# Performance work log

Measured on AMD Instinct MI355X. Metric: run time of the kernel, lower is better.

## Reference

```python
import jax, jax.numpy as jnp
import numpy as np

DIM = 768
HEADS = 12
HEAD_DIM = DIM // HEADS


def setup_inputs() -> dict:
    key = jax.random.key(0)
    ks = jax.random.split(key, 5)
    B, S = 4, 2048
    init = 0.02
    x = jax.random.normal(ks[0], (B, S, DIM), dtype=jnp.float32)
    w_qkv = jax.random.normal(ks[1], (DIM, 3 * DIM), dtype=jnp.float32) * init
    b_qkv = jnp.zeros((3 * DIM,), dtype=jnp.float32)
    w_out = jax.random.normal(ks[2], (DIM, DIM), dtype=jnp.float32) * init
    b_out = jnp.zeros((DIM,), dtype=jnp.float32)
    return {"x": x, "w_qkv": w_qkv, "b_qkv": b_qkv, "w_out": w_out, "b_out": b_out}


def reference(x, w_qkv, b_qkv, w_out, b_out):
    B, S, D = x.shape
    # QKV projection: [B,S,3D] -> [3,B,H,S,hd]
    qkv = x @ w_qkv + b_qkv
    qkv = qkv.reshape(B, S, 3, HEADS, HEAD_DIM).transpose(2, 0, 3, 1, 4)
    q, k, v = qkv[0], qkv[1], qkv[2]
    # NOTE: original scales by 1/sqrt(head_num), not 1/sqrt(head_dim)
    scale = 1.0 / jnp.sqrt(jnp.float32(HEADS))
    scores = jnp.einsum("bhqd,bhkd->bhqk", q, k) * scale
    attn = jax.nn.softmax(scores, axis=-1)
    out = jnp.einsum("bhqk,bhkd->bhqd", attn, v)
    out = out.transpose(0, 2, 1, 3).reshape(B, S, D)
    return out @ w_out + b_out
```

## Files before the change

kernel.cpp:

```cpp
#include <hip/hip_runtime.h>
#include <hip/hip_bf16.h>
#include <cstdint>
#include <cstddef>

#define HEADS 12
#define HD    64
#define NB    4
#define SEQ   2048
#define DIM   768
#define NQKV  2304

static constexpr float QSCALE = 0.2886751345948129f * 1.4426950408889634f;

typedef __attribute__((ext_vector_type(8))) short short8;
typedef __attribute__((ext_vector_type(4))) short short4v;
typedef __attribute__((ext_vector_type(4))) float f32x4;

__device__ inline unsigned short f2bf(float x) {
    union { float f; uint32_t u; } v; v.f = x;
    return (unsigned short)((v.u + 0x7fffu + ((v.u >> 16) & 1u)) >> 16);
}

__device__ inline unsigned short f2bf_fast(float x) {
    __hip_bfloat16 h = __float2bfloat16(x);
    unsigned short u;
    __builtin_memcpy(&u, &h, 2);
    return u;
}

__device__ inline void gld16(const void* g, void* l) {
    __builtin_amdgcn_global_load_lds(
        (const __attribute__((address_space(1))) unsigned int*)g,
        (__attribute__((address_space(3))) unsigned int*)l, 16, 0, 0);
}

__device__ inline void transpose_tile(
    const float* __restrict__ w, unsigned short* __restrict__ wT,
    int ncols, int nrows, int bx, int by, float (*tile)[65])
{
    const int k0 = by * 64;
    const int n0 = bx * 64;
    const int tr = threadIdx.x >> 4;
    const int tc4 = (threadIdx.x & 15) * 4;
    #pragma unroll
    for (int it = 0; it < 4; ++it) {
        const int kk = tr + it * 16;
        *reinterpret_cast<float4*>(&tile[kk][tc4]) =
            *reinterpret_cast<const float4*>(w + (size_t)(k0 + kk) * ncols + n0 + tc4);
    }
    __syncthreads();
    #pragma unroll
    for (int it = 0; it < 4; ++it) {
        const int nn = tr + it * 16;
        short4v o;
        #pragma unroll
        for (int r = 0; r < 4; ++r) o[r] = (short)f2bf(tile[tc4 + r][nn]);
        *reinterpret_cast<short4v*>(wT + (size_t)(n0 + nn) * nrows + k0 + tc4) = o;
    }
}

__global__ __launch_bounds__(256) void prep_kernel(
    const float* __restrict__ x, unsigned short* __restrict__ xb,
    const float* __restrict__ wq, unsigned short* __restrict__ wqT,
    const float* __restrict__ wo, unsigned short* __restrict__ woT)
{
    __shared__ float tile[64][65];
    const int bid = blockIdx.x;
    if (bid < 3072) {
        const size_t i = ((size_t)bid * 256 + threadIdx.x) * 8;
        const float4 a = *reinterpret_cast<const float4*>(x + i);
        const float4 b = *reinterpret_cast<const float4*>(x + i + 4);
        short8 o;
        o[0] = (short)f2bf(a.x); o[1] = (short)f2bf(a.y);
        o[2] = (short)f2bf(a.z); o[3] = (short)f2bf(a.w);
        o[4] = (short)f2bf(b.x); o[5] = (short)f2bf(b.y);
        o[6] = (short)f2bf(b.z); o[7] = (short)f2bf(b.w);
        *reinterpret_cast<short8*>(xb + i) = o;
    } else if (bid < 3072 + 432) {
        const int r = bid - 3072;
        transpose_tile(wq, wqT, NQKV, DIM, r % 36, r / 36, tile);
    } else {
        const int r = bid - 3504;
        transpose_tile(wo, woT, DIM, DIM, r % 12, r / 12, tile);
    }
}

__global__ __launch_bounds__(512) void qkv_gemm_bf16(
    const unsigned short* __restrict__ A,
    const unsigned short* __restrict__ BT,
    const float* __restrict__ bias,
    unsigned short* __restrict__ qb, unsigned short* __restrict__ kb,
    unsigned short* __restrict__ vt)
{
    __shared__ __align__(16) unsigned short As[2][128][64];
    __shared__ __align__(16) unsigned short Bs[2][128][64];

    const int tid = threadIdx.x;
    const int wave = tid >> 6;
    const int lane = tid & 63;
    const int col = lane & 15;
    const int g = lane >> 4;
    const int m0 = blockIdx.y * 128;
    const int n0 = blockIdx.x * 128;
    const int wr = wave >> 2;
    const int wc = wave & 3;

    f32x4 acc[4][2] = {};

    auto STAGE = [&](int kt, int bsel) {
        #pragma unroll
        for (int it = 0; it < 2; ++it) {
            const int slot = tid + it * 512;
            const int row = slot >> 3;
            const int cg = (slot & 7) ^ (row & 7);
            gld16(A + (size_t)(m0 + row) * DIM + kt + cg * 8,
                  &As[bsel][0][0] + (size_t)slot * 8);
            gld16(BT + (size_t)(n0 + row) * DIM + kt + cg * 8,
                  &Bs[bsel][0][0] + (size_t)slot * 8);
        }
    };

    const int NKT = DIM / 64;
    STAGE(0, 0);
    asm volatile("s_waitcnt vmcnt(0)" ::: "memory");
    __builtin_amdgcn_s_barrier();

    for (int t = 0; t < NKT; ++t) {
        const int cur = t & 1;
        if (t + 1 < NKT) STAGE((t + 1) * 64, cur ^ 1);

        #pragma unroll
        for (int ks = 0; ks < 2; ++ks) {
            short8 af[4], bf[2];
            #pragma unroll
            for (int i = 0; i < 4; ++i) {
                const int ra = wr * 64 + i * 16 + col;
                af[i] = *reinterpret_cast<const short8*>(
                    &As[cur][ra][(((ks * 4 + g) ^ (ra & 7)) << 3)]);
            }
            #pragma unroll
            for (int j = 0; j < 2; ++j) {
                const int rb = wc * 32 + j * 16 + col;
                bf[j] = *reinterpret_cast<const short8*>(
                    &Bs[cur][rb][(((ks * 4 + g) ^ (rb & 7)) << 3)]);
            }
            #pragma unroll
            for (int i = 0; i < 4; ++i)
                #pragma unroll
                for (int j = 0; j < 2; ++j)
                    acc[i][j] = __builtin_amdgcn_mfma_f32_16x16x32_bf16(
                        af[i], bf[j], acc[i][j], 0, 0, 0);
        }

        if (t + 1 < NKT) {
            asm volatile("s_waitcnt vmcnt(0)" ::: "memory");
            __builtin_amdgcn_s_barrier();
        }
    }

    const int which = n0 / DIM;
    #pragma unroll
    for (int j = 0; j < 2; ++j) {
        const int n = n0 + wc * 32 + j * 16 + col;
        const int rem = n - which * DIM;
        const int h = rem >> 6, dh = rem & 63;
        const float bj = bias[n];
        #pragma unroll
        for (int i = 0; i < 4; ++i) {
            const int mbase = m0 + wr * 64 + i * 16 + g * 4;
            const int b_ = mbase >> 11;
            const int s_ = mbase & 2047;
            const size_t bh = (size_t)(b_ * HEADS + h);
            if (which == 2) {
                short4v pk;
                #pragma unroll
                for (int r = 0; r < 4; ++r)
                    pk[r] = (short)f2bf(acc[i][j][r] + bj);
                *reinterpret_cast<short4v*>(vt + (bh * HD + dh) * SEQ + s_) = pk;
            } else {
                unsigned short* dst = (which == 0) ? qb : kb;
                const float sc = (which == 0) ? QSCALE : 1.0f;
                #pragma unroll
                for (int r = 0; r < 4; ++r)
                    dst[(bh * SEQ + s_ + r) * HD + dh] =
                        f2bf((acc[i][j][r] + bj) * sc);
            }
        }
    }
}

__global__ __launch_bounds__(512) void attn_kernel(
    const unsigned short* __restrict__ qb, const unsigned short* __restrict__ kbuf,
    const unsigned short* __restrict__ vt, unsigned short* __restrict__ ctxb)
{
    __shared__ __align__(16) unsigned short Ks[2][64][64];
    __shared__ __align__(16) unsigned short Vs[2][64][64];
    __shared__ __align__(16) unsigned short Ps[8][16][64];

    const int tid = threadIdx.x;
    const int wave = tid >> 6;
    const int lane = tid & 63;
    const int col = lane & 15;
    const int g   = lane >> 4;

    const int bid = blockIdx.x;
    const int vbid = (bid & 7) * 96 + (bid >> 3);
    const int bh = vbid >> 4;
    const int q0 = (vbid & 15) * 128;
    const int wq = q0 + wave * 16 + col;

    const size_t hb = (size_t)bh * SEQ * HD;

    short8 qf[2];
    {
        const unsigned short* src = qb + hb + (size_t)wq * HD + g * 8;
        qf[0] = *reinterpret_cast<const short8*>(src);
        qf[1] = *reinterpret_cast<const short8*>(src + 32);
    }

    f32x4 acc4[4] = {};
    float l_part = 0.0f;

    const unsigned short* Kg = kbuf + hb;
    const unsigned short* Vg = vt + hb;

    const int srow = tid >> 3;
    const int scl  = tid & 7;
    const int scg  = scl ^ (srow & 7);

    auto STAGE = [&](int jt, int bsel) {
        const int kb0 = jt * 64;
        gld16(Kg + (size_t)(kb0 + srow) * HD + scg * 8,
              &Ks[bsel][0][0] + (size_t)tid * 8);
        gld16(Vg + (size_t)srow * SEQ + kb0 + scg * 8,
              &Vs[bsel][0][0] + (size_t)tid * 8);
    };

    const int NT = SEQ / 64;
    STAGE(0, 0);

    for (int jt = 0; jt < NT; ++jt) {
        const int cur = jt & 1;
        if (jt + 1 < NT) {
            STAGE(jt + 1, cur ^ 1);
            asm volatile("s_waitcnt vmcnt(2)" ::: "memory");
        } else {
            asm volatile("s_waitcnt vmcnt(0)" ::: "memory");
        }
        __builtin_amdgcn_s_barrier();

        f32x4 st[4] = {};
        __builtin_amdgcn_s_setprio(1);
        #pragma unroll
        for (int m = 0; m < 4; ++m) {
            const int row = m * 16 + col;
            const short8 kf0 = *reinterpret_cast<const short8*>(
                &Ks[cur][row][((g ^ (row & 7)) << 3)]);
            const short8 kf1 = *reinterpret_cast<const short8*>(
                &Ks[cur][row][(((g + 4) ^ (row & 7)) << 3)]);
            st[m] = __builtin_amdgcn_mfma_f32_16x16x32_bf16(kf0, qf[0], st[m], 0, 0, 0);
            st[m] = __builtin_amdgcn_mfma_f32_16x16x32_bf16(kf1, qf[1], st[m], 0, 0, 0);
        }
        __builtin_amdgcn_s_setprio(0);

        float s0 = 0.0f, s1 = 0.0f, s2 = 0.0f, s3 = 0.0f;
        #pragma unroll
        for (int m = 0; m < 4; ++m) {
            float p[4];
            p[0] = __builtin_amdgcn_exp2f(st[m][0]);
            p[1] = __builtin_amdgcn_exp2f(st[m][1]);
            p[2] = __builtin_amdgcn_exp2f(st[m][2]);
            p[3] = __builtin_amdgcn_exp2f(st[m][3]);
            s0 += p[0]; s1 += p[1]; s2 += p[2]; s3 += p[3];
            short4v pk;
            #pragma unroll
            for (int r = 0; r < 4; ++r) pk[r] = (short)f2bf_fast(p[r]);
            const int scw = (2 * m + (g >> 1)) ^ (col & 7);
            *reinterpret_cast<short4v*>(
                &Ps[wave][col][(scw << 3) + ((g & 1) << 2)]) = pk;
        }
        l_part += (s0 + s1) + (s2 + s3);

        const short8 pf0 = *reinterpret_cast<const short8*>(
            &Ps[wave][col][((g ^ (col & 7)) << 3)]);
        const short8 pf1 = *reinterpret_cast<const short8*>(
            &Ps[wave][col][(((g + 4) ^ (col & 7)) << 3)]);

        __builtin_amdgcn_s_setprio(1);
        #pragma unroll
        for (int nb = 0; nb < 4; ++nb) {
            const int row = nb * 16 + col;
            const short8 vf0 = *reinterpret_cast<const short8*>(
                &Vs[cur][row][((g ^ (row & 7)) << 3)]);
            const short8 vf1 = *reinterpret_cast<const short8*>(
                &Vs[cur][row][(((g + 4) ^ (row & 7)) << 3)]);
            acc4[nb] = __builtin_amdgcn_mfma_f32_16x16x32_bf16(pf0, vf0, acc4[nb], 0, 0, 0);
            acc4[nb] = __builtin_amdgcn_mfma_f32_16x16x32_bf16(pf1, vf1, acc4[nb], 0, 0, 0);
        }
        __builtin_amdgcn_s_setprio(0);

        __builtin_amdgcn_s_barrier();
    }

    float lt = l_part + __shfl_xor(l_part, 16);
    lt += __shfl_xor(lt, 32);
    float lr[4];
    #pragma unroll
    for (int r = 0; r < 4; ++r) lr[r] = 1.0f / __shfl(lt, g * 4 + r);
    const int b_ = bh / HEADS;
    const int h = bh - b_ * HEADS;
    #pragma unroll
    for (int nb = 0; nb < 4; ++nb)
        #pragma unroll
        for (int r = 0; r < 4; ++r) {
            const int s_ = q0 + wave * 16 + g * 4 + r;
            ctxb[((size_t)b_ * SEQ + s_) * DIM + h * HD + nb * 16 + col] =
                f2bf_fast(acc4[nb][r] * lr[r]);
        }
}

__global__ __launch_bounds__(512) void out_gemm_bf16(
    const unsigned short* __restrict__ A,
    const unsigned short* __restrict__ BT,
    const float* __restrict__ bias, float* __restrict__ out)
{
    __shared__ __align__(16) unsigned short As[2][128][64];
    __shared__ __align__(16) unsigned short Bs[2][128][64];

    const int tid = threadIdx.x;
    const int wave = tid >> 6;
    const int lane = tid & 63;
    const int col = lane & 15;
    const int g = lane >> 4;
    const int m0 = blockIdx.y * 128;
    const int n0 = blockIdx.x * 128;
    const int wr = wave >> 2;
    const int wc = wave & 3;

    f32x4 acc[4][2] = {};

    auto STAGE = [&](int kt, int bsel) {
        #pragma unroll
        for (int it = 0; it < 2; ++it) {
            const int slot = tid + it * 512;
            const int row = slot >> 3;
            const int cg = (slot & 7) ^ (row & 7);
            gld16(A + (size_t)(m0 + row) * DIM + kt + cg * 8,
                  &As[bsel][0][0] + (size_t)slot * 8);
            gld16(BT + (size_t)(n0 + row) * DIM + kt + cg * 8,
                  &Bs[bsel][0][0] + (size_t)slot * 8);
        }
    };

    const int NKT = DIM / 64;
    STAGE(0, 0);
    asm volatile("s_waitcnt vmcnt(0)" ::: "memory");
    __builtin_amdgcn_s_barrier();

    for (int t = 0; t < NKT; ++t) {
        const int cur = t & 1;
        if (t + 1 < NKT) STAGE((t + 1) * 64, cur ^ 1);

        #pragma unroll
        for (int ks = 0; ks < 2; ++ks) {
            short8 af[4], bf[2];
            #pragma unroll
            for (int i = 0; i < 4; ++i) {
                const int ra = wr * 64 + i * 16 + col;
                af[i] = *reinterpret_cast<const short8*>(
                    &As[cur][ra][(((ks * 4 + g) ^ (ra & 7)) << 3)]);
            }
            #pragma unroll
            for (int j = 0; j < 2; ++j) {
                const int rb = wc * 32 + j * 16 + col;
                bf[j] = *reinterpret_cast<const short8*>(
                    &Bs[cur][rb][(((ks * 4 + g) ^ (rb & 7)) << 3)]);
            }
            #pragma unroll
            for (int i = 0; i < 4; ++i)
                #pragma unroll
                for (int j = 0; j < 2; ++j)
                    acc[i][j] = __builtin_amdgcn_mfma_f32_16x16x32_bf16(
                        af[i], bf[j], acc[i][j], 0, 0, 0);
        }

        if (t + 1 < NKT) {
            asm volatile("s_waitcnt vmcnt(0)" ::: "memory");
            __builtin_amdgcn_s_barrier();
        }
    }

    #pragma unroll
    for (int j = 0; j < 2; ++j) {
        const int n = n0 + wc * 32 + j * 16 + col;
        const float bj = bias[n];
        #pragma unroll
        for (int i = 0; i < 4; ++i) {
            const int m = m0 + wr * 64 + i * 16 + g * 4;
            #pragma unroll
            for (int r = 0; r < 4; ++r)
                out[(size_t)(m + r) * DIM + n] = acc[i][j][r] + bj;
        }
    }
}

extern "C" void kernel_launch(void* const* d_in, const int* in_sizes, int n_in,
                              void* d_out, int out_size, void* d_ws, size_t ws_size,
                              hipStream_t stream)
{
    const float* x     = (const float*)d_in[0];
    const float* w_qkv = (const float*)d_in[1];
    const float* b_qkv = (const float*)d_in[2];
    const float* w_out = (const float*)d_in[3];
    const float* b_out = (const float*)d_in[4];
    float* out = (float*)d_out;

    const size_t QSZ = (size_t)NB * HEADS * SEQ * HD;
    unsigned short* qb   = (unsigned short*)d_ws;
    unsigned short* kb   = qb + QSZ;
    unsigned short* vt   = kb + QSZ;
    unsigned short* xb   = vt + QSZ;
    unsigned short* ctxb = xb + QSZ;
    unsigned short* wqT  = ctxb + QSZ;
    unsigned short* woT  = wqT + (size_t)NQKV * DIM;

    prep_kernel<<<3648, 256, 0, stream>>>(x, xb, w_qkv, wqT, w_out, woT);
    qkv_gemm_bf16<<<dim3(NQKV / 128, (NB * SEQ) / 128), 512, 0, stream>>>(
        xb, wqT, b_qkv, qb, kb, vt);
    attn_kernel<<<dim3((SEQ / 128) * NB * HEADS), 512, 0, stream>>>(qb, kb, vt, ctxb);
    out_gemm_bf16<<<dim3(DIM / 128, (NB * SEQ) / 128), 512, 0, stream>>>(
        ctxb, woT, b_out, out);
}
```

Baseline: 148.6 us.

## Remap GEMM blocks for XCD locality and compute softmax row sums via MFMA

Both GEMMs now use a 1D grid, and the block index is remapped so that consecutive blocks on each XCD share the same weight column tile (n0) and walk along M. This targets better L2 reuse per chiplet. In the attention kernel, the per-lane scalar accumulation of exp values and the final shuffle reduction are replaced by an extra pair of MFMAs against an all-ones bf16 vector, producing row sums directly in the accumulator layout. This trades two MFMAs per tile for removed VALU adds and shuffles, and the row sums are now taken from the bf16-rounded P values.

```diff
diff --git a/kernel.cpp b/kernel.cpp
--- a/kernel.cpp
+++ b/kernel.cpp
@@ -100,8 +100,10 @@
     const int lane = tid & 63;
     const int col = lane & 15;
     const int g = lane >> 4;
-    const int m0 = blockIdx.y * 128;
-    const int n0 = blockIdx.x * 128;
+    const int bid = blockIdx.x;
+    const int vbid = (bid & 7) * 144 + (bid >> 3);
+    const int n0 = (vbid / 64) * 128;
+    const int m0 = (vbid % 64) * 128;
     const int wr = wave >> 2;
     const int wc = wave & 3;
 
@@ -218,8 +220,11 @@
         qf[1] = *reinterpret_cast<const short8*>(src + 32);
     }
 
+    const short ONE = (short)0x3F80;
+    const short8 ONES = {ONE, ONE, ONE, ONE, ONE, ONE, ONE, ONE};
+
     f32x4 acc4[4] = {};
-    float l_part = 0.0f;
+    f32x4 acc5 = {};
 
     const unsigned short* Kg = kbuf + hb;
     const unsigned short* Vg = vt + hb;
@@ -263,7 +268,6 @@
         }
         __builtin_amdgcn_s_setprio(0);
 
-        float s0 = 0.0f, s1 = 0.0f, s2 = 0.0f, s3 = 0.0f;
         #pragma unroll
         for (int m = 0; m < 4; ++m) {
             float p[4];
@@ -271,7 +275,6 @@
             p[1] = __builtin_amdgcn_exp2f(st[m][1]);
             p[2] = __builtin_amdgcn_exp2f(st[m][2]);
             p[3] = __builtin_amdgcn_exp2f(st[m][3]);
-            s0 += p[0]; s1 += p[1]; s2 += p[2]; s3 += p[3];
             short4v pk;
             #pragma unroll
             for (int r = 0; r < 4; ++r) pk[r] = (short)f2bf_fast(p[r]);
@@ -279,7 +282,6 @@
             *reinterpret_cast<short4v*>(
                 &Ps[wave][col][(scw << 3) + ((g & 1) << 2)]) = pk;
         }
-        l_part += (s0 + s1) + (s2 + s3);
 
         const short8 pf0 = *reinterpret_cast<const short8*>(
             &Ps[wave][col][((g ^ (col & 7)) << 3)]);
@@ -297,16 +299,16 @@
             acc4[nb] = __builtin_amdgcn_mfma_f32_16x16x32_bf16(pf0, vf0, acc4[nb], 0, 0, 0);
             acc4[nb] = __builtin_amdgcn_mfma_f32_16x16x32_bf16(pf1, vf1, acc4[nb], 0, 0, 0);
         }
+        acc5 = __builtin_amdgcn_mfma_f32_16x16x32_bf16(pf0, ONES, acc5, 0, 0, 0);
+        acc5 = __builtin_amdgcn_mfma_f32_16x16x32_bf16(pf1, ONES, acc5, 0, 0, 0);
         __builtin_amdgcn_s_setprio(0);
 
         __builtin_amdgcn_s_barrier();
     }
 
-    float lt = l_part + __shfl_xor(l_part, 16);
-    lt += __shfl_xor(lt, 32);
     float lr[4];
     #pragma unroll
-    for (int r = 0; r < 4; ++r) lr[r] = 1.0f / __shfl(lt, g * 4 + r);
+    for (int r = 0; r < 4; ++r) lr[r] = 1.0f / acc5[r];
     const int b_ = bh / HEADS;
     const int h = bh - b_ * HEADS;
     #pragma unroll
@@ -332,8 +334,10 @@
     const int lane = tid & 63;
     const int col = lane & 15;
     const int g = lane >> 4;
-    const int m0 = blockIdx.y * 128;
-    const int n0 = blockIdx.x * 128;
+    const int bid = blockIdx.x;
+    const int vbid = (bid & 7) * 48 + (bid >> 3);
+    const int n0 = (vbid / 64) * 128;
+    const int m0 = (vbid % 64) * 128;
     const int wr = wave >> 2;
     const int wc = wave & 3;
 
@@ -425,9 +429,7 @@
     unsigned short* woT  = wqT + (size_t)NQKV * DIM;
 
     prep_kernel<<<3648, 256, 0, stream>>>(x, xb, w_qkv, wqT, w_out, woT);
-    qkv_gemm_bf16<<<dim3(NQKV / 128, (NB * SEQ) / 128), 512, 0, stream>>>(
-        xb, wqT, b_qkv, qb, kb, vt);
+    qkv_gemm_bf16<<<dim3(1152), 512, 0, stream>>>(xb, wqT, b_qkv, qb, kb, vt);
     attn_kernel<<<dim3((SEQ / 128) * NB * HEADS), 512, 0, stream>>>(qb, kb, vt, ctxb);
-    out_gemm_bf16<<<dim3(DIM / 128, (NB * SEQ) / 128), 512, 0, stream>>>(
-        ctxb, woT, b_out, out);
-}
+    out_gemm_bf16<<<dim3(384), 512, 0, stream>>>(ctxb, woT, b_out, out);
+}
```

After: 155.3 us. +4.5%, slower.
